# Optimization experiments

Measured on AMD Instinct MI355X. Metric: run time of the kernel, lower is better.

The kernel has to match this reference:

```python
import jax, jax.numpy as jnp
import numpy as np


def setup_inputs() -> dict:
    key = jax.random.key(0)
    ks = jax.random.split(key, 8)
    B, L, U, D = 256, 16, 512, 2
    x = jax.random.randint(ks[0], (B, L, L), 0, D, dtype=jnp.int32)
    def s(k, shape, fan):
        return jax.random.normal(k, shape, jnp.float32) / np.float32(np.sqrt(fan))
    return {
        "x": x,
        "W_in_h": s(ks[1], (D, U), D),
        "W_in_v": s(ks[2], (D, U), D),
        "W_carry_h": s(ks[3], (U, U), U),
        "b_carry_h": jnp.zeros((U,), jnp.float32),
        "W_carry_v": s(ks[4], (U, U), U),
        "W_out": s(ks[5], (U, D), U),
        "b_out": jnp.zeros((D,), jnp.float32),
    }


def reference(x, W_in_h, W_in_v, W_carry_h, b_carry_h, W_carry_v, W_out, b_out):
    B, L = x.shape[0], x.shape[1]
    U = W_carry_h.shape[0]
    D = W_out.shape[1]

    # one-hot spins, padded: zero row above, zero columns left/right
    oh = jax.nn.one_hot(jnp.transpose(x, (1, 2, 0)), D, dtype=jnp.float32)  # (L,L,B,D)
    inputs = jnp.zeros((L + 1, L + 2, B, D), jnp.float32).at[1:, 1:-1].set(oh)
    direction = jnp.where(jnp.arange(L) % 2 == 0, 1, -1)  # boustrophedon row flips

    def rev(line, d):
        return jnp.where(d == 1, line, jnp.flip(line, 0))

    def cell(h, xs):
        xh, xv, cv = xs  # left one-hot (B,D), above one-hot (B,D), above hidden (B,U)
        new = jax.nn.elu(xh @ W_in_h + xv @ W_in_v + h @ W_carry_h + b_carry_h + cv @ W_carry_v)
        p = jax.nn.softmax(new @ W_out + b_out)  # (B,D)
        return new, (new, p)

    def row(states, xs):
        cur, prev, d = xs  # (L+2,B,D), (L+2,B,D), scalar direction
        cur_r, prev_r, st_r = rev(cur, d), rev(prev, d), rev(states, d)
        _, (new_states, probs) = jax.lax.scan(
            cell, jnp.zeros((B, U), jnp.float32),
            (cur_r[:-2], prev_r[1:-1], st_r))
        logp = jnp.log(jnp.sum(probs * cur_r[1:-1], axis=2))  # (L,B)
        return rev(new_states, d), jnp.sum(logp, axis=0)

    _, prob = jax.lax.scan(row, jnp.zeros((L, B, U), jnp.float32),
                           (inputs[1:], inputs[:-1], direction))
    return jnp.nan_to_num(jnp.sum(prob, axis=0))  # (B,) log-probabilities
```

## Files before the change

kernel.cpp:

```cpp
#include <hip/hip_runtime.h>
#include <hip/hip_bf16.h>
#include <math.h>

#define Bsz 256
#define Lsz 16
#define Usz 512
#define BPW 2
#define NWG (Bsz / BPW)
#define NT  512

typedef __attribute__((ext_vector_type(8))) short bf16x8;
typedef __attribute__((ext_vector_type(4))) float f32x4;

__device__ __forceinline__ unsigned short f2bf(float f) {
    union { __hip_bfloat16 h; unsigned short s; } u;
    u.h = __float2bfloat16(f);
    return u.s;
}

__device__ __forceinline__ int st_off(int row, int k) {
    return row * Usz + ((k & 504) ^ ((row & 7) << 3)) + (k & 7);
}

__global__ void conv_frag(const float* __restrict__ Wa, const float* __restrict__ Wb,
                          unsigned int* __restrict__ outa, unsigned int* __restrict__ outb) {
    const int bid  = blockIdx.x;
    const float* W        = (bid < 512) ? Wa : Wb;
    unsigned int* out     = (bid < 512) ? outa : outb;
    const int tile = bid & 511;
    const int l    = threadIdx.x;
    const int kb = tile >> 5, ub = tile & 31;
    const int k0 = kb * 32 + (l >> 4) * 8;
    const int u  = ub * 16 + (l & 15);
    unsigned v[4];
    #pragma unroll
    for (int p = 0; p < 4; ++p) {
        unsigned lo = f2bf(W[(size_t)(k0 + 2 * p) * Usz + u]);
        unsigned hi = f2bf(W[(size_t)(k0 + 2 * p + 1) * Usz + u]);
        v[p] = lo | (hi << 16);
    }
    *(uint4*)(out + (size_t)(tile * 64 + l) * 4) = make_uint4(v[0], v[1], v[2], v[3]);
}

__global__ __launch_bounds__(NT, 2) void rnn2d_v3(
    const int*   __restrict__ x,
    const float* __restrict__ Wih,
    const float* __restrict__ Wiv,
    const float* __restrict__ bch,
    const float* __restrict__ Wout,
    const float* __restrict__ bout,
    const unsigned int* __restrict__ wchf,
    const unsigned int* __restrict__ wcvf,
    float*       __restrict__ out)
{
    __shared__ __attribute__((aligned(16))) unsigned short stm[32 * Usz];
    __shared__ float Vb[32 * Usz];
    __shared__ __attribute__((aligned(16))) unsigned short hb[2][2][Usz];
    __shared__ __attribute__((aligned(16))) unsigned short zc[8];
    __shared__ float wihA[2][Usz], wivA[2][Usz], bcA[Usz], woA[Usz][2];
    __shared__ float wred[2][8][2][2];
    __shared__ float logp[2];

    const int tid = threadIdx.x;
    const int b0  = blockIdx.x * BPW;
    const int w   = tid >> 6;
    const int l   = tid & 63;
    const int r   = l & 15;
    const int hi4 = l >> 4;

    if (tid < 2) logp[tid] = 0.f;
    if (tid < 8) zc[tid] = 0;
    for (int idx = tid; idx < 32 * Usz; idx += NT) Vb[idx] = 0.f;
    wihA[0][tid] = Wih[tid];  wihA[1][tid] = Wih[Usz + tid];
    wivA[0][tid] = Wiv[tid];  wivA[1][tid] = Wiv[Usz + tid];
    bcA[tid] = bch[tid];
    woA[tid][0] = Wout[2 * tid];  woA[tid][1] = Wout[2 * tid + 1];
    const float bo0 = bout[0], bo1 = bout[1];

    const bf16x8* __restrict__ WF = (const bf16x8*)wchf;
    const bf16x8* __restrict__ VF = (const bf16x8*)wcvf;
    bf16x8 wreg[32];
    #pragma unroll
    for (int kb = 0; kb < 16; ++kb) {
        wreg[2 * kb]     = WF[(kb * 32 + w * 4 + 0) * 64 + l];
        wreg[2 * kb + 1] = WF[(kb * 32 + w * 4 + 1) * 64 + l];
    }

    int p = 0;
    for (int i = 0; i < Lsz; ++i) {
        const int dir = (i & 1) ? -1 : 1;

        if (i > 0) {
            f32x4 vacc[2][4];
            #pragma unroll
            for (int m = 0; m < 2; ++m)
                #pragma unroll
                for (int t4 = 0; t4 < 4; ++t4) vacc[m][t4] = (f32x4)(0.f);
            const int kl = hi4 * 8;
            for (int kb = 0; kb < 16; ++kb) {
                const int ka = kb * 32 + kl;
                bf16x8 A0 = *(const bf16x8*)&stm[st_off(r,      ka)];
                bf16x8 A1 = *(const bf16x8*)&stm[st_off(r + 16, ka)];
                #pragma unroll
                for (int t4 = 0; t4 < 4; ++t4) {
                    bf16x8 Bf = VF[(size_t)(kb * 32 + w * 4 + t4) * 64 + l];
                    vacc[0][t4] = __builtin_amdgcn_mfma_f32_16x16x32_bf16(A0, Bf, vacc[0][t4], 0, 0, 0);
                    vacc[1][t4] = __builtin_amdgcn_mfma_f32_16x16x32_bf16(A1, Bf, vacc[1][t4], 0, 0, 0);
                }
            }
            #pragma unroll
            for (int m = 0; m < 2; ++m)
                #pragma unroll
                for (int t4 = 0; t4 < 4; ++t4)
                    #pragma unroll
                    for (int q = 0; q < 4; ++q) {
                        const int row = m * 16 + hi4 * 4 + q;
                        const int uc  = (w * 4 + t4) * 16 + r;
                        Vb[row * Usz + uc] = vacc[m][t4][q];
                    }
        }

        for (int idx = tid; idx < 2 * 2 * Usz; idx += NT)
            ((unsigned short*)hb)[idx] = 0;
        __syncthreads();

        for (int t = 0; t < Lsz; ++t) {
            const int c = (dir == 1) ? t : (Lsz - 1 - t);

            f32x4 acc0 = (f32x4)(0.f), acc1 = (f32x4)(0.f),
                  acc2 = (f32x4)(0.f), acc3 = (f32x4)(0.f);
            bf16x8 sbuf[16];
            #pragma unroll
            for (int kb = 0; kb < 16; ++kb)
                sbuf[kb] = WF[(kb * 32 + w * 4 + 2) * 64 + l];
            #pragma unroll
            for (int kb = 0; kb < 16; ++kb) {
                const bf16x8 Af = (r < 2)
                    ? *(const bf16x8*)&hb[p][r][((kb * 4 + hi4) ^ r) << 3]
                    : *(const bf16x8*)zc;
                acc0 = __builtin_amdgcn_mfma_f32_16x16x32_bf16(Af, wreg[2 * kb],     acc0, 0, 0, 0);
                acc1 = __builtin_amdgcn_mfma_f32_16x16x32_bf16(Af, wreg[2 * kb + 1], acc1, 0, 0, 0);
                acc2 = __builtin_amdgcn_mfma_f32_16x16x32_bf16(Af, sbuf[kb],         acc2, 0, 0, 0);
            }
            #pragma unroll
            for (int kb = 0; kb < 16; ++kb)
                sbuf[kb] = WF[(kb * 32 + w * 4 + 3) * 64 + l];
            #pragma unroll
            for (int kb = 0; kb < 16; ++kb) {
                const bf16x8 Af = (r < 2)
                    ? *(const bf16x8*)&hb[p][r][((kb * 4 + hi4) ^ r) << 3]
                    : *(const bf16x8*)zc;
                acc3 = __builtin_amdgcn_mfma_f32_16x16x32_bf16(Af, sbuf[kb], acc3, 0, 0, 0);
            }

            const int  cl   = c - dir;
            const bool hasL = (t > 0);
            const bool hasV = (i > 0);
            if (l < 16) {
                const int sl0 = hasL ? x[(b0 + 0) * 256 + i * 16 + cl]      : 0;
                const int sv0 = hasV ? x[(b0 + 0) * 256 + (i - 1) * 16 + c] : 0;
                const int sl1 = hasL ? x[(b0 + 1) * 256 + i * 16 + cl]      : 0;
                const int sv1 = hasV ? x[(b0 + 1) * 256 + (i - 1) * 16 + c] : 0;
                float lp00 = 0.f, lp01 = 0.f, lp10 = 0.f, lp11 = 0.f;

                #define EPI(ACC, TQ) { \
                    const int u = w * 64 + (TQ) * 16 + l; \
                    float v0 = (ACC)[0] + Vb[(c * 2 + 0) * Usz + u] + bcA[u]; \
                    float v1 = (ACC)[1] + Vb[(c * 2 + 1) * Usz + u] + bcA[u]; \
                    if (hasL) { v0 += wihA[sl0][u]; v1 += wihA[sl1][u]; } \
                    if (hasV) { v0 += wivA[sv0][u]; v1 += wivA[sv1][u]; } \
                    v0 = v0 > 0.f ? v0 : expm1f(v0); \
                    v1 = v1 > 0.f ? v1 : expm1f(v1); \
                    hb[p ^ 1][0][(((u >> 3) ^ 0) << 3) | (u & 7)] = f2bf(v0); \
                    hb[p ^ 1][1][(((u >> 3) ^ 1) << 3) | (u & 7)] = f2bf(v1); \
                    stm[st_off(c * 2 + 0, u)] = f2bf(v0); \
                    stm[st_off(c * 2 + 1, u)] = f2bf(v1); \
                    lp00 += v0 * woA[u][0];  lp01 += v0 * woA[u][1]; \
                    lp10 += v1 * woA[u][0];  lp11 += v1 * woA[u][1]; }

                EPI(acc0, 0)
                EPI(acc1, 1)
                EPI(acc2, 2)
                EPI(acc3, 3)
                #undef EPI

                #pragma unroll
                for (int off = 8; off; off >>= 1) {
                    lp00 += __shfl_down(lp00, off);
                    lp01 += __shfl_down(lp01, off);
                    lp10 += __shfl_down(lp10, off);
                    lp11 += __shfl_down(lp11, off);
                }
                if (l == 0) {
                    wred[t & 1][w][0][0] = lp00;  wred[t & 1][w][0][1] = lp01;
                    wred[t & 1][w][1][0] = lp10;  wred[t & 1][w][1][1] = lp11;
                }
            }
            __syncthreads();

            if (tid < 2) {
                float g0 = bo0, g1 = bo1;
                #pragma unroll
                for (int ww = 0; ww < 8; ++ww) {
                    g0 += wred[t & 1][ww][tid][0];
                    g1 += wred[t & 1][ww][tid][1];
                }
                const int   sc = x[(b0 + tid) * 256 + i * 16 + c];
                const float m  = fmaxf(g0, g1);
                const float lse = m + logf(expf(g0 - m) + expf(g1 - m));
                logp[tid] += (sc ? g1 : g0) - lse;
            }
            p ^= 1;
        }
    }

    if (tid < 2) {
        float v = logp[tid];
        if (isnan(v)) v = 0.f;
        else if (isinf(v)) v = v > 0.f ? 3.4028235e38f : -3.4028235e38f;
        out[b0 + tid] = v;
    }
}

extern "C" void kernel_launch(void* const* d_in, const int* in_sizes, int n_in,
                              void* d_out, int out_size, void* d_ws, size_t ws_size,
                              hipStream_t stream) {
    const int*   x    = (const int*)  d_in[0];
    const float* Wih  = (const float*)d_in[1];
    const float* Wiv  = (const float*)d_in[2];
    const float* Wch  = (const float*)d_in[3];
    const float* bch  = (const float*)d_in[4];
    const float* Wcv  = (const float*)d_in[5];
    const float* Wout = (const float*)d_in[6];
    const float* bout = (const float*)d_in[7];

    unsigned int* ws_wch = (unsigned int*)d_ws;
    unsigned int* ws_wcv = (unsigned int*)((char*)d_ws + 512 * 1024);

    conv_frag<<<1024, 64, 0, stream>>>(Wch, Wcv, ws_wch, ws_wcv);
    rnn2d_v3<<<NWG, NT, 0, stream>>>(x, Wih, Wiv, bch, Wout, bout,
                                     ws_wch, ws_wcv, (float*)d_out);
}
```

Measured before the change: 2.229 ms.

## Keep recurrent weights in registers and LDS, parallelize epilogue across threads

Part of the third weight column block is now cached in LDS, and the remaining fragments are prefetched into a rotating register array that is refilled during MFMA work. Before, all of this was reloaded from global memory every cell. The epilogue now spreads over all 512 threads through a partial-sum buffer instead of only 16 lanes per wave. The vertical buffer is stored as bf16, and x values are staged in LDS once per row. Plain barriers are replaced with lgkmcnt-wait barriers, and the log-softmax is computed redundantly per thread. The costs are extra register pressure, bf16 rounding of the vertical contribution, and more complex, fragile k-block scheduling.

```diff
diff --git a/kernel.cpp b/kernel.cpp
--- a/kernel.cpp
+++ b/kernel.cpp
@@ -2,12 +2,8 @@
 #include <hip/hip_bf16.h>
 #include <math.h>
 
-#define Bsz 256
-#define Lsz 16
-#define Usz 512
-#define BPW 2
-#define NWG (Bsz / BPW)
 #define NT  512
+#define NWG 128
 
 typedef __attribute__((ext_vector_type(8))) short bf16x8;
 typedef __attribute__((ext_vector_type(4))) float f32x4;
@@ -17,16 +13,22 @@
     u.h = __float2bfloat16(f);
     return u.s;
 }
-
+__device__ __forceinline__ float bf2f(unsigned short s) {
+    union { float f; unsigned u; } v; v.u = ((unsigned)s) << 16; return v.f;
+}
 __device__ __forceinline__ int st_off(int row, int k) {
-    return row * Usz + ((k & 504) ^ ((row & 7) << 3)) + (k & 7);
+    return row * 512 + ((k & 504) ^ ((row & 7) << 3)) + (k & 7);
+}
+__device__ __forceinline__ void barL() {
+    asm volatile("s_waitcnt lgkmcnt(0)" ::: "memory");
+    __builtin_amdgcn_s_barrier();
 }
 
 __global__ void conv_frag(const float* __restrict__ Wa, const float* __restrict__ Wb,
                           unsigned int* __restrict__ outa, unsigned int* __restrict__ outb) {
-    const int bid  = blockIdx.x;
-    const float* W        = (bid < 512) ? Wa : Wb;
-    unsigned int* out     = (bid < 512) ? outa : outb;
+    const int bid = blockIdx.x;
+    const float* W    = (bid < 512) ? Wa : Wb;
+    unsigned int* out = (bid < 512) ? outa : outb;
     const int tile = bid & 511;
     const int l    = threadIdx.x;
     const int kb = tile >> 5, ub = tile & 31;
@@ -35,14 +37,16 @@
     unsigned v[4];
     #pragma unroll
     for (int p = 0; p < 4; ++p) {
-        unsigned lo = f2bf(W[(size_t)(k0 + 2 * p) * Usz + u]);
-        unsigned hi = f2bf(W[(size_t)(k0 + 2 * p + 1) * Usz + u]);
+        unsigned lo = f2bf(W[(size_t)(k0 + 2 * p) * 512 + u]);
+        unsigned hi = f2bf(W[(size_t)(k0 + 2 * p + 1) * 512 + u]);
         v[p] = lo | (hi << 16);
     }
     *(uint4*)(out + (size_t)(tile * 64 + l) * 4) = make_uint4(v[0], v[1], v[2], v[3]);
 }
 
-__global__ __launch_bounds__(NT, 2) void rnn2d_v3(
+#define MFMA(A, B, C) __builtin_amdgcn_mfma_f32_16x16x32_bf16((A), (B), (C), 0, 0, 0)
+
+__global__ __launch_bounds__(NT, 2) void rnn2d_v4(
     const int*   __restrict__ x,
     const float* __restrict__ Wih,
     const float* __restrict__ Wiv,
@@ -53,41 +57,51 @@
     const unsigned int* __restrict__ wcvf,
     float*       __restrict__ out)
 {
-    __shared__ __attribute__((aligned(16))) unsigned short stm[32 * Usz];
-    __shared__ float Vb[32 * Usz];
-    __shared__ __attribute__((aligned(16))) unsigned short hb[2][2][Usz];
-    __shared__ __attribute__((aligned(16))) unsigned short zc[8];
-    __shared__ float wihA[2][Usz], wivA[2][Usz], bcA[Usz], woA[Usz][2];
-    __shared__ float wred[2][8][2][2];
-    __shared__ float logp[2];
+    __shared__ __attribute__((aligned(16))) bf16x8        wlds[8 * 10 * 64];
+    __shared__ __attribute__((aligned(16))) unsigned short stm[32 * 512];
+    __shared__ __attribute__((aligned(16))) unsigned short Vb[32 * 512];
+    __shared__ __attribute__((aligned(16))) unsigned short hb[2][2][512];
+    __shared__ __attribute__((aligned(16))) float          part[512 * 2];
+    __shared__ int    xc[2][2][16];
+    __shared__ float4 wred[2][8];
 
     const int tid = threadIdx.x;
-    const int b0  = blockIdx.x * BPW;
-    const int w   = tid >> 6;
-    const int l   = tid & 63;
-    const int r   = l & 15;
-    const int hi4 = l >> 4;
-
-    if (tid < 2) logp[tid] = 0.f;
-    if (tid < 8) zc[tid] = 0;
-    for (int idx = tid; idx < 32 * Usz; idx += NT) Vb[idx] = 0.f;
-    wihA[0][tid] = Wih[tid];  wihA[1][tid] = Wih[Usz + tid];
-    wivA[0][tid] = Wiv[tid];  wivA[1][tid] = Wiv[Usz + tid];
-    bcA[tid] = bch[tid];
-    woA[tid][0] = Wout[2 * tid];  woA[tid][1] = Wout[2 * tid + 1];
-    const float bo0 = bout[0], bo1 = bout[1];
+    const int b0  = blockIdx.x * 2;
+    const int w   = tid >> 6, l = tid & 63;
+    const int r   = l & 15,  hi4 = l >> 4, rb = r & 1;
+
+    const float wih0 = Wih[tid], wih1 = Wih[512 + tid];
+    const float wiv0 = Wiv[tid], wiv1 = Wiv[512 + tid];
+    const float bc   = bch[tid];
+    const float wo0  = Wout[2 * tid], wo1 = Wout[2 * tid + 1];
+    const float bo0  = bout[0],       bo1 = bout[1];
 
     const bf16x8* __restrict__ WF = (const bf16x8*)wchf;
     const bf16x8* __restrict__ VF = (const bf16x8*)wcvf;
+
+    for (int idx = tid; idx < 32 * 512 / 2; idx += NT) {
+        ((unsigned*)stm)[idx] = 0;
+        ((unsigned*)Vb)[idx]  = 0;
+    }
+
     bf16x8 wreg[32];
     #pragma unroll
     for (int kb = 0; kb < 16; ++kb) {
         wreg[2 * kb]     = WF[(kb * 32 + w * 4 + 0) * 64 + l];
         wreg[2 * kb + 1] = WF[(kb * 32 + w * 4 + 1) * 64 + l];
     }
-
+    #pragma unroll
+    for (int f = 0; f < 10; ++f)
+        wlds[(w * 10 + f) * 64 + l] = WF[(f * 32 + w * 4 + 2) * 64 + l];
+    bf16x8 S[11];
+    #pragma unroll
+    for (int j = 0; j < 11; ++j)
+        S[j] = WF[((j < 6) ? ((10 + j) * 32 + w * 4 + 2) : ((j - 6) * 32 + w * 4 + 3)) * 64 + l];
+
+    float logp0 = 0.f, logp1 = 0.f;
     int p = 0;
-    for (int i = 0; i < Lsz; ++i) {
+
+    for (int i = 0; i < 16; ++i) {
         const int dir = (i & 1) ? -1 : 1;
 
         if (i > 0) {
@@ -104,8 +118,8 @@
                 #pragma unroll
                 for (int t4 = 0; t4 < 4; ++t4) {
                     bf16x8 Bf = VF[(size_t)(kb * 32 + w * 4 + t4) * 64 + l];
-                    vacc[0][t4] = __builtin_amdgcn_mfma_f32_16x16x32_bf16(A0, Bf, vacc[0][t4], 0, 0, 0);
-                    vacc[1][t4] = __builtin_amdgcn_mfma_f32_16x16x32_bf16(A1, Bf, vacc[1][t4], 0, 0, 0);
+                    vacc[0][t4] = MFMA(A0, Bf, vacc[0][t4]);
+                    vacc[1][t4] = MFMA(A1, Bf, vacc[1][t4]);
                 }
             }
             #pragma unroll
@@ -113,109 +127,126 @@
                 #pragma unroll
                 for (int t4 = 0; t4 < 4; ++t4)
                     #pragma unroll
-                    for (int q = 0; q < 4; ++q) {
-                        const int row = m * 16 + hi4 * 4 + q;
-                        const int uc  = (w * 4 + t4) * 16 + r;
-                        Vb[row * Usz + uc] = vacc[m][t4][q];
-                    }
+                    for (int q = 0; q < 4; ++q)
+                        Vb[(m * 16 + hi4 * 4 + q) * 512 + (w * 4 + t4) * 16 + r] =
+                            f2bf(vacc[m][t4][q]);
+            #pragma unroll
+            for (int j = 0; j < 11; ++j)
+                S[j] = WF[((j < 6) ? ((10 + j) * 32 + w * 4 + 2)
+                                   : ((j - 6) * 32 + w * 4 + 3)) * 64 + l];
         }
 
-        for (int idx = tid; idx < 2 * 2 * Usz; idx += NT)
-            ((unsigned short*)hb)[idx] = 0;
+        if (tid < 64) {
+            const int b = tid >> 5, rs = (tid >> 4) & 1, c = tid & 15;
+            int v = 0;
+            if (rs == 0)      v = x[(b0 + b) * 256 + i * 16 + c];
+            else if (i > 0)   v = x[(b0 + b) * 256 + (i - 1) * 16 + c];
+            xc[b][rs][c] = v;
+        }
+        ((unsigned*)hb)[tid] = 0;
         __syncthreads();
 
-        for (int t = 0; t < Lsz; ++t) {
-            const int c = (dir == 1) ? t : (Lsz - 1 - t);
+        for (int t = 0; t < 16; ++t) {
+            const int c = (dir == 1) ? t : 15 - t;
 
             f32x4 acc0 = (f32x4)(0.f), acc1 = (f32x4)(0.f),
                   acc2 = (f32x4)(0.f), acc3 = (f32x4)(0.f);
-            bf16x8 sbuf[16];
-            #pragma unroll
-            for (int kb = 0; kb < 16; ++kb)
-                sbuf[kb] = WF[(kb * 32 + w * 4 + 2) * 64 + l];
-            #pragma unroll
-            for (int kb = 0; kb < 16; ++kb) {
-                const bf16x8 Af = (r < 2)
-                    ? *(const bf16x8*)&hb[p][r][((kb * 4 + hi4) ^ r) << 3]
-                    : *(const bf16x8*)zc;
-                acc0 = __builtin_amdgcn_mfma_f32_16x16x32_bf16(Af, wreg[2 * kb],     acc0, 0, 0, 0);
-                acc1 = __builtin_amdgcn_mfma_f32_16x16x32_bf16(Af, wreg[2 * kb + 1], acc1, 0, 0, 0);
-                acc2 = __builtin_amdgcn_mfma_f32_16x16x32_bf16(Af, sbuf[kb],         acc2, 0, 0, 0);
-            }
-            #pragma unroll
-            for (int kb = 0; kb < 16; ++kb)
-                sbuf[kb] = WF[(kb * 32 + w * 4 + 3) * 64 + l];
-            #pragma unroll
-            for (int kb = 0; kb < 16; ++kb) {
-                const bf16x8 Af = (r < 2)
-                    ? *(const bf16x8*)&hb[p][r][((kb * 4 + hi4) ^ r) << 3]
-                    : *(const bf16x8*)zc;
-                acc3 = __builtin_amdgcn_mfma_f32_16x16x32_bf16(Af, sbuf[kb], acc3, 0, 0, 0);
-            }
+
+            #define AF(KB) (*(const bf16x8*)&hb[p][rb][(((KB) * 4 + hi4) ^ rb) << 3])
+
+            #pragma unroll
+            for (int kb = 0; kb < 5; ++kb) {
+                bf16x8 Af = AF(kb);
+                acc0 = MFMA(Af, wreg[2 * kb],     acc0);
+                acc1 = MFMA(Af, wreg[2 * kb + 1], acc1);
+                acc3 = MFMA(Af, S[6 + kb],        acc3);
+            }
+            #pragma unroll
+            for (int kb = 10; kb < 16; ++kb) {
+                bf16x8 Af = AF(kb);
+                acc0 = MFMA(Af, wreg[2 * kb],     acc0);
+                acc1 = MFMA(Af, wreg[2 * kb + 1], acc1);
+                acc2 = MFMA(Af, S[kb - 10],       acc2);
+            }
+            #pragma unroll
+            for (int j = 0; j < 11; ++j)
+                S[j] = WF[((5 + j) * 32 + w * 4 + 3) * 64 + l];
+            #pragma unroll
+            for (int kb = 0; kb < 10; ++kb) {
+                bf16x8 Af = AF(kb);
+                bf16x8 Bw = wlds[(w * 10 + kb) * 64 + l];
+                acc2 = MFMA(Af, Bw, acc2);
+                if (kb >= 5) {
+                    acc0 = MFMA(Af, wreg[2 * kb],     acc0);
+                    acc1 = MFMA(Af, wreg[2 * kb + 1], acc1);
+                }
+            }
+            #pragma unroll
+            for (int kb = 5; kb < 16; ++kb) {
+                bf16x8 Af = AF(kb);
+                acc3 = MFMA(Af, S[kb - 5], acc3);
+            }
+            if (t < 15) {
+                #pragma unroll
+                for (int j = 0; j < 11; ++j)
+                    S[j] = WF[((j < 6) ? ((10 + j) * 32 + w * 4 + 2)
+                                       : ((j - 6) * 32 + w * 4 + 3)) * 64 + l];
+            }
+            #undef AF
+
+            if (l < 16) {
+                *(float2*)&part[(w * 64 +  0 + l) * 2] = make_float2(acc0[0], acc0[1]);
+                *(float2*)&part[(w * 64 + 16 + l) * 2] = make_float2(acc1[0], acc1[1]);
+                *(float2*)&part[(w * 64 + 32 + l) * 2] = make_float2(acc2[0], acc2[1]);
+                *(float2*)&part[(w * 64 + 48 + l) * 2] = make_float2(acc3[0], acc3[1]);
+            }
+            barL();
 
             const int  cl   = c - dir;
             const bool hasL = (t > 0);
             const bool hasV = (i > 0);
-            if (l < 16) {
-                const int sl0 = hasL ? x[(b0 + 0) * 256 + i * 16 + cl]      : 0;
-                const int sv0 = hasV ? x[(b0 + 0) * 256 + (i - 1) * 16 + c] : 0;
-                const int sl1 = hasL ? x[(b0 + 1) * 256 + i * 16 + cl]      : 0;
-                const int sv1 = hasV ? x[(b0 + 1) * 256 + (i - 1) * 16 + c] : 0;
-                float lp00 = 0.f, lp01 = 0.f, lp10 = 0.f, lp11 = 0.f;
-
-                #define EPI(ACC, TQ) { \
-                    const int u = w * 64 + (TQ) * 16 + l; \
-                    float v0 = (ACC)[0] + Vb[(c * 2 + 0) * Usz + u] + bcA[u]; \
-                    float v1 = (ACC)[1] + Vb[(c * 2 + 1) * Usz + u] + bcA[u]; \
-                    if (hasL) { v0 += wihA[sl0][u]; v1 += wihA[sl1][u]; } \
-                    if (hasV) { v0 += wivA[sv0][u]; v1 += wivA[sv1][u]; } \
-                    v0 = v0 > 0.f ? v0 : expm1f(v0); \
-                    v1 = v1 > 0.f ? v1 : expm1f(v1); \
-                    hb[p ^ 1][0][(((u >> 3) ^ 0) << 3) | (u & 7)] = f2bf(v0); \
-                    hb[p ^ 1][1][(((u >> 3) ^ 1) << 3) | (u & 7)] = f2bf(v1); \
-                    stm[st_off(c * 2 + 0, u)] = f2bf(v0); \
-                    stm[st_off(c * 2 + 1, u)] = f2bf(v1); \
-                    lp00 += v0 * woA[u][0];  lp01 += v0 * woA[u][1]; \
-                    lp10 += v1 * woA[u][0];  lp11 += v1 * woA[u][1]; }
-
-                EPI(acc0, 0)
-                EPI(acc1, 1)
-                EPI(acc2, 2)
-                EPI(acc3, 3)
-                #undef EPI
-
-                #pragma unroll
-                for (int off = 8; off; off >>= 1) {
-                    lp00 += __shfl_down(lp00, off);
-                    lp01 += __shfl_down(lp01, off);
-                    lp10 += __shfl_down(lp10, off);
-                    lp11 += __shfl_down(lp11, off);
-                }
-                if (l == 0) {
-                    wred[t & 1][w][0][0] = lp00;  wred[t & 1][w][0][1] = lp01;
-                    wred[t & 1][w][1][0] = lp10;  wred[t & 1][w][1][1] = lp11;
-                }
-            }
-            __syncthreads();
-
-            if (tid < 2) {
-                float g0 = bo0, g1 = bo1;
-                #pragma unroll
-                for (int ww = 0; ww < 8; ++ww) {
-                    g0 += wred[t & 1][ww][tid][0];
-                    g1 += wred[t & 1][ww][tid][1];
-                }
-                const int   sc = x[(b0 + tid) * 256 + i * 16 + c];
-                const float m  = fmaxf(g0, g1);
-                const float lse = m + logf(expf(g0 - m) + expf(g1 - m));
-                logp[tid] += (sc ? g1 : g0) - lse;
+            const float2 pa = *(const float2*)&part[tid * 2];
+            float v0 = pa.x + bf2f(Vb[(c * 2 + 0) * 512 + tid]) + bc;
+            float v1 = pa.y + bf2f(Vb[(c * 2 + 1) * 512 + tid]) + bc;
+            if (hasL) { v0 += xc[0][0][cl] ? wih1 : wih0;  v1 += xc[1][0][cl] ? wih1 : wih0; }
+            if (hasV) { v0 += xc[0][1][c]  ? wiv1 : wiv0;  v1 += xc[1][1][c]  ? wiv1 : wiv0; }
+            v0 = v0 > 0.f ? v0 : expm1f(v0);
+            v1 = v1 > 0.f ? v1 : expm1f(v1);
+            hb[p ^ 1][0][(((tid >> 3) ^ 0) << 3) | (tid & 7)] = f2bf(v0);
+            hb[p ^ 1][1][(((tid >> 3) ^ 1) << 3) | (tid & 7)] = f2bf(v1);
+            stm[st_off(c * 2 + 0, tid)] = f2bf(v0);
+            stm[st_off(c * 2 + 1, tid)] = f2bf(v1);
+            const int sc0 = xc[0][0][c], sc1 = xc[1][0][c];
+            float lp0 = v0 * wo0, lp1 = v0 * wo1, lp2 = v1 * wo0, lp3 = v1 * wo1;
+            #pragma unroll
+            for (int off = 32; off; off >>= 1) {
+                lp0 += __shfl_down(lp0, off);
+                lp1 += __shfl_down(lp1, off);
+                lp2 += __shfl_down(lp2, off);
+                lp3 += __shfl_down(lp3, off);
+            }
+            if (l == 0) wred[t & 1][w] = make_float4(lp0, lp1, lp2, lp3);
+            barL();
+
+            float g00 = bo0, g01 = bo1, g10 = bo0, g11 = bo1;
+            #pragma unroll
+            for (int ww = 0; ww < 8; ++ww) {
+                const float4 v4 = wred[t & 1][ww];
+                g00 += v4.x;  g01 += v4.y;  g10 += v4.z;  g11 += v4.w;
+            }
+            {
+                const float m0 = fmaxf(g00, g01), m1 = fmaxf(g10, g11);
+                const float ls0 = m0 + log1pf(expf(fminf(g00, g01) - m0));
+                const float ls1 = m1 + log1pf(expf(fminf(g10, g11) - m1));
+                logp0 += (sc0 ? g01 : g00) - ls0;
+                logp1 += (sc1 ? g11 : g10) - ls1;
             }
             p ^= 1;
         }
     }
 
     if (tid < 2) {
-        float v = logp[tid];
+        float v = tid ? logp1 : logp0;
         if (isnan(v)) v = 0.f;
         else if (isinf(v)) v = v > 0.f ? 3.4028235e38f : -3.4028235e38f;
         out[b0 + tid] = v;
@@ -238,6 +269,6 @@
     unsigned int* ws_wcv = (unsigned int*)((char*)d_ws + 512 * 1024);
 
     conv_frag<<<1024, 64, 0, stream>>>(Wch, Wcv, ws_wch, ws_wcv);
-    rnn2d_v3<<<NWG, NT, 0, stream>>>(x, Wih, Wiv, bch, Wout, bout,
+    rnn2d_v4<<<NWG, NT, 0, stream>>>(x, Wih, Wiv, bch, Wout, bout,
                                      ws_wch, ws_wcv, (float*)d_out);
 }
```

Result: slower. 2.693 ms (+20.8%).
